# Optimization experiments

Hardware: AMD Instinct MI355X
Metric: run time of the kernel (lower is better)

The kernel has to match this reference:

```python
import jax, jax.numpy as jnp
import numpy as np

LN_EPS = 1e-9

def _layer_norm(x, g, b):
    mu = jnp.mean(x, axis=-1, keepdims=True)
    var = jnp.mean((x - mu) ** 2, axis=-1, keepdims=True)
    return (x - mu) * jax.lax.rsqrt(var + LN_EPS) * g + b

def _ffn(x, w1, b1, w2, b2, ln_g, ln_b):
    h = jax.nn.gelu(x @ w1 + b1, approximate=False)
    h = h @ w2 + b2
    return _layer_norm(h, ln_g, ln_b)

def _kernel_mean(x, y):
    d = x.shape[1]
    x2 = jnp.sum(x * x, axis=1)[:, None]
    y2 = jnp.sum(y * y, axis=1)[None, :]
    sq = x2 + y2 - 2.0 * (x @ y.T)  # [Nx, Ny]
    return jnp.mean(jnp.exp(-sq / (d * d)))

def _mmd(x, y):
    return _kernel_mean(x, x) + _kernel_mean(y, y) - 2.0 * _kernel_mean(x, y)

def setup_inputs() -> dict:
    key = jax.random.key(0)
    ks = jax.random.split(key, 8)
    B, S, D, DI, DL = 8, 512, 1024, 4096, 64
    s = lambda fan: 1.0 / np.sqrt(fan)
    return {
        "hidden": jax.random.normal(ks[0], (B, S, D), jnp.float32),
        "true_samples": jax.random.normal(ks[1], (B * S, DL), jnp.float32),
        "enc_w1": jax.random.normal(ks[2], (D, DI), jnp.float32) * s(D),
        "enc_b1": jnp.zeros((DI,), jnp.float32),
        "enc_w2": jax.random.normal(ks[3], (DI, DL), jnp.float32) * s(DI),
        "enc_b2": jnp.zeros((DL,), jnp.float32),
        "enc_ln_g": jnp.ones((DL,), jnp.float32),
        "enc_ln_b": jnp.zeros((DL,), jnp.float32),
        "dec_w1": jax.random.normal(ks[4], (DL, DI), jnp.float32) * s(DL),
        "dec_b1": jnp.zeros((DI,), jnp.float32),
        "dec_w2": jax.random.normal(ks[5], (DI, D), jnp.float32) * s(DI),
        "dec_b2": jnp.zeros((D,), jnp.float32),
        "dec_ln_g": jnp.ones((D,), jnp.float32),
        "dec_ln_b": jnp.zeros((D,), jnp.float32),
    }

def reference(hidden, true_samples, enc_w1, enc_b1, enc_w2, enc_b2, enc_ln_g, enc_ln_b,
              dec_w1, dec_b1, dec_w2, dec_b2, dec_ln_g, dec_ln_b):
    latent = _ffn(hidden, enc_w1, enc_b1, enc_w2, enc_b2, enc_ln_g, enc_ln_b)  # [B,S,DL]
    recon = _ffn(latent, dec_w1, dec_b1, dec_w2, dec_b2, dec_ln_g, dec_ln_b)   # [B,S,D]
    B, S, DL = latent.shape
    lat_flat = latent.reshape(-1, DL)  # [B*S, DL]
    reg_loss = _mmd(true_samples, lat_flat) / B * S
    return recon, latent, reg_loss
```

## Files before the change

kernel.cpp:

```cpp
#include <hip/hip_runtime.h>
#include <hip/hip_bf16.h>
#include <math.h>


typedef __attribute__((ext_vector_type(8))) short short8;
typedef __attribute__((ext_vector_type(4))) float float4a;
typedef __attribute__((ext_vector_type(4))) unsigned short us4;

__device__ inline ushort bf16r(float x) {
    union { float f; unsigned u; } c; c.f = x;
    unsigned r = (c.u + 0x7fffu + ((c.u >> 16) & 1u)) >> 16;
    return (ushort)r;
}

__device__ inline void gld_lds16(const void* g, void* l) {
    __builtin_amdgcn_global_load_lds(
        (const __attribute__((address_space(1))) void*)g,
        (__attribute__((address_space(3))) void*)l, 16, 0, 0);
}

template <int N> __device__ inline void wait_vmcnt() {
    if constexpr (N == 0) asm volatile("s_waitcnt vmcnt(0)" ::: "memory");
    else if constexpr (N == 4) asm volatile("s_waitcnt vmcnt(4)" ::: "memory");
    else if constexpr (N == 6) asm volatile("s_waitcnt vmcnt(6)" ::: "memory");
}

__device__ inline float fast_gelu(float v) {
    float v2 = v * v;
    float u = v * __builtin_fmaf(0.07135481627f, v2, 1.5957691216f);
    u = fminf(u, 30.0f);
    float e = __expf(u);
    return v * e * __builtin_amdgcn_rcpf(e + 1.0f);
}

__global__ __launch_bounds__(256) void k_pre(
        const float* __restrict__ hidden, ushort* __restrict__ A1bf,
        const float* __restrict__ tsamp, ushort* __restrict__ Tbf,
        float* __restrict__ sq_t, float* __restrict__ acc,
        const float* __restrict__ i0, ushort* __restrict__ o0,
        const float* __restrict__ i1, ushort* __restrict__ o1,
        const float* __restrict__ i2, ushort* __restrict__ o2,
        const float* __restrict__ i3, ushort* __restrict__ o3) {
    int b = blockIdx.x, tid = threadIdx.x;
    if (b == 0 && tid < 24) acc[tid] = 0.0f;
    if (b < 4096) {
        int i = b * 1024 + tid * 4;
        float4 v = *(const float4*)(hidden + i);
        us4 o = {bf16r(v.x), bf16r(v.y), bf16r(v.z), bf16r(v.w)};
        *(us4*)(A1bf + i) = o;
        return;
    }
    if (b < 4352) {
        int i = (b - 4096) * 1024 + tid * 4;
        float4 v = *(const float4*)(tsamp + i);
        us4 o = {bf16r(v.x), bf16r(v.y), bf16r(v.z), bf16r(v.w)};
        *(us4*)(Tbf + i) = o;
        float s = v.x * v.x + v.y * v.y + v.z * v.z + v.w * v.w;
#pragma unroll
        for (int off = 8; off; off >>= 1) s += __shfl_xor(s, off);
        if ((tid & 15) == 0) sq_t[i >> 6] = s;
        return;
    }
    __shared__ float t[32][33];
    const float* in; ushort* out; int R, C, lb;
    if (b < 8448)      { in = i0; out = o0; R = 1024; C = 4096; lb = b - 4352; }
    else if (b < 8704) { in = i1; out = o1; R = 4096; C = 64;   lb = b - 8448; }
    else if (b < 8960) { in = i2; out = o2; R = 64;   C = 4096; lb = b - 8704; }
    else               { in = i3; out = o3; R = 4096; C = 1024; lb = b - 8960; }
    int bx = (lb % (C / 32)) * 32;
    int by = (lb / (C / 32)) * 32;
    int tx = tid & 31, ty = tid >> 5;
#pragma unroll
    for (int i = 0; i < 32; i += 8)
        t[ty + i][tx] = in[(size_t)(by + ty + i) * C + (bx + tx)];
    __syncthreads();
#pragma unroll
    for (int i = 0; i < 32; i += 8)
        out[(size_t)(bx + ty + i) * R + (by + tx)] = bf16r(t[tx][ty + i]);
}

template <int BN, int EPI, bool SWZ>
__global__ __launch_bounds__(256) void k_gemm(
        const ushort* __restrict__ A, const ushort* __restrict__ Bt,
        const float* __restrict__ bias, void* __restrict__ Out,
        float* __restrict__ Out2, int M, int N, int K, int KC) {
    constexpr int BM = 128, BK = 64;
    constexpr int WAVES_N = BN / 64;
    constexpr int WAVES_M = 4 / WAVES_N;
    constexpr int WM = BM / WAVES_M;
    constexpr int MT = WM / 16;
    constexpr int NT = 4;
    constexpr int CA = BM / 32, CB = BN / 32;

    __shared__ ushort sA[BM * 64];
    __shared__ ushort sB[BN * 64];

    const int tid  = threadIdx.x;
    const int wave = tid >> 6, lane = tid & 63;
    const int wm = wave / WAVES_N, wn = wave % WAVES_N;
    int bx = blockIdx.x, by = blockIdx.y;
    if constexpr (SWZ) {
        int lin = blockIdx.x + gridDim.x * blockIdx.y;
        by = lin % gridDim.y;
        bx = lin / gridDim.y;
    }
    const int m0 = by * BM, n0 = bx * BN;
    const int lrow = lane & 15, lq = lane >> 4;
    const int srow8 = lane >> 3;
    const int sk8   = lane & 7;
    const int kbeg = blockIdx.z * KC;

    const ushort* pA[CA]; unsigned lA[CA];
#pragma unroll
    for (int j = 0; j < CA; ++j) {
        int c = wave * CA + j;
        int r = c * 8 + srow8;
        pA[j] = &A[(size_t)(m0 + r) * K + kbeg + ((sk8 ^ (r & 7)) * 8)];
        lA[j] = c * 512;
    }
    const ushort* pB[CB]; unsigned lB[CB];
#pragma unroll
    for (int j = 0; j < CB; ++j) {
        int c = wave * CB + j;
        int r = c * 8 + srow8;
        pB[j] = &Bt[(size_t)(n0 + r) * K + kbeg + ((sk8 ^ (r & 7)) * 8)];
        lB[j] = c * 512;
    }
    unsigned aoff[2][MT], boff[2][NT];
#pragma unroll
    for (int h = 0; h < 2; ++h) {
#pragma unroll
        for (int mt = 0; mt < MT; ++mt) {
            int r = wm * WM + mt * 16 + lrow;
            aoff[h][mt] = r * 64 + (((h * 4 + lq) ^ (r & 7)) * 8);
        }
#pragma unroll
        for (int nt = 0; nt < NT; ++nt) {
            int r = wn * 64 + nt * 16 + lrow;
            boff[h][nt] = r * 64 + (((h * 4 + lq) ^ (r & 7)) * 8);
        }
    }

    float4a acc[MT][NT];
#pragma unroll
    for (int mt = 0; mt < MT; ++mt)
#pragma unroll
        for (int nt = 0; nt < NT; ++nt)
            acc[mt][nt] = (float4a){0.f, 0.f, 0.f, 0.f};

    for (int k0 = 0; k0 < KC; k0 += BK) {
#pragma unroll
        for (int j = 0; j < CA; ++j) {
            gld_lds16(pA[j], &sA[lA[j]]);
            pA[j] += BK;
        }
#pragma unroll
        for (int j = 0; j < CB; ++j) {
            gld_lds16(pB[j], &sB[lB[j]]);
            pB[j] += BK;
        }
        __syncthreads();
#pragma unroll
        for (int h = 0; h < 2; ++h) {
            short8 af[MT], bfr[NT];
#pragma unroll
            for (int mt = 0; mt < MT; ++mt)
                af[mt] = *(short8*)(&sA[aoff[h][mt]]);
#pragma unroll
            for (int nt = 0; nt < NT; ++nt)
                bfr[nt] = *(short8*)(&sB[boff[h][nt]]);
#pragma unroll
            for (int mt = 0; mt < MT; ++mt)
#pragma unroll
                for (int nt = 0; nt < NT; ++nt)
                    acc[mt][nt] = __builtin_amdgcn_mfma_f32_16x16x32_bf16(
                        af[mt], bfr[nt], acc[mt][nt], 0, 0, 0);
        }
        __syncthreads();
    }

    float* dstp = nullptr;
    if constexpr (EPI == 2) {
        if (Out2 && blockIdx.z) dstp = Out2;
        else dstp = (float*)Out + (size_t)blockIdx.z * M * N;
    }
#pragma unroll
    for (int mt = 0; mt < MT; ++mt)
#pragma unroll
        for (int nt = 0; nt < NT; ++nt) {
            int col = n0 + wn * 64 + nt * 16 + lrow;
            float bv = 0.f;
            if constexpr (EPI != 2) bv = bias[col];
#pragma unroll
            for (int r = 0; r < 4; ++r) {
                int row = m0 + wm * WM + mt * 16 + lq * 4 + r;
                float v = acc[mt][nt][r] + bv;
                if constexpr (EPI == 0) {
                    ((ushort*)Out)[(size_t)row * N + col] = bf16r(fast_gelu(v));
                } else if constexpr (EPI == 1) {
                    ((float*)Out)[(size_t)row * N + col] = v;
                } else {
                    dstp[(size_t)row * N + col] = v;
                }
            }
        }
}

template <int BN, int EPI, int CX, int CY>
__global__ __launch_bounds__(512, 2) void k_gemm256(
        const ushort* __restrict__ A, const ushort* __restrict__ Bt,
        const float* __restrict__ bias, void* __restrict__ Out,
        float* __restrict__ Out2, int M, int N, int K, int KC) {
    constexpr int BM = 256, BK = 64;
    constexpr int AI = 4;
    constexpr int BI = BN / 64;
    constexpr int BLO = (BN == 256) ? 2 : 0;
    constexpr int WAVES_N = BN / 64;
    constexpr int WAVES_M = 8 / WAVES_N;
    constexpr int WM = BM / WAVES_M;
    constexpr int MT = WM / 16;
    constexpr int NT = 4;
    constexpr int PH = MT / 2;
    constexpr int INF = AI + BLO;

    __shared__ ushort sA[2][BM * 64];
    __shared__ ushort sB[2][BN * 64];

    const int tid = threadIdx.x;
    const int wave = tid >> 6, lane = tid & 63;
    const int wm = wave / WAVES_N, wn = wave % WAVES_N;

    const int gx = gridDim.x, gy = gridDim.y;
    const int lin = blockIdx.x + gx * (blockIdx.y + gy * blockIdx.z);
    const int nwg = gx * gy * gridDim.z;
    const int cpx = nwg >> 3;
    const int swz = (lin & 7) * cpx + (lin >> 3);
    const int nz  = gx * gy;
    const int zz  = swz / nz;
    const int rr  = swz % nz;
    const int chunk = rr / (CX * CY);
    const int lcl   = rr % (CX * CY);
    const int ncx   = gx / CX;
    const int bx = (chunk % ncx) * CX + (lcl % CX);
    const int by = (chunk / ncx) * CY + (lcl / CX);

    const int m0 = by * BM, n0 = bx * BN;
    const int lrow = lane & 15, lq = lane >> 4;
    const int kbeg = zz * KC;
    const int nT = KC / BK;

    const int crow = tid >> 3;
    const int ck8  = (tid & 7) ^ (crow & 7);
    const ushort* pAbase = A  + (size_t)(m0 + crow) * K + kbeg + ck8 * 8;
    const ushort* pBbase = Bt + (size_t)(n0 + crow) * K + kbeg + ck8 * 8;

    const int a0  = (wm * WM + lrow) * 64;
    const int b0  = (wn * 64 + lrow) * 64;
    const int sw0 = ((lq) ^ (lrow & 7)) * 8;
    const int sw1 = ((4 + lq) ^ (lrow & 7)) * 8;

    float4a acc[MT][NT];
#pragma unroll
    for (int mt = 0; mt < MT; ++mt)
#pragma unroll
        for (int nt = 0; nt < NT; ++nt)
            acc[mt][nt] = (float4a){0.f, 0.f, 0.f, 0.f};

#pragma unroll
    for (int j = 0; j < AI; ++j)
        gld_lds16(pAbase + (size_t)j * 64 * K, &sA[0][j * 4096 + wave * 512]);
#pragma unroll
    for (int j = 0; j < BI; ++j)
        gld_lds16(pBbase + (size_t)j * 64 * K, &sB[0][j * 4096 + wave * 512]);
    if (nT > 1) {
#pragma unroll
        for (int j = 0; j < AI; ++j)
            gld_lds16(pAbase + (size_t)j * 64 * K + BK,
                      &sA[1][j * 4096 + wave * 512]);
#pragma unroll
        for (int j = 0; j < BLO; ++j)
            gld_lds16(pBbase + (size_t)j * 64 * K + BK,
                      &sB[1][j * 4096 + wave * 512]);
        wait_vmcnt<INF>();
    } else {
        wait_vmcnt<0>();
    }
    __builtin_amdgcn_s_barrier();
    __builtin_amdgcn_sched_barrier(0);

    short8 bfr[2][NT];

    for (int t = 0; t < nT; ++t) {
        const int d = t & 1;
        const bool pf1 = (t + 1 < nT), pf2 = (t + 2 < nT);
        const size_t koff1 = (size_t)(t + 1) * BK;
        const size_t koff2 = (size_t)(t + 2) * BK;

#pragma unroll
        for (int q = 0; q < PH; ++q) {
            short8 af[2][2];
#pragma unroll
            for (int i = 0; i < 2; ++i) {
                af[0][i] = *(const short8*)(&sA[d][a0 + (q * 2 + i) * 1024 + sw0]);
                af[1][i] = *(const short8*)(&sA[d][a0 + (q * 2 + i) * 1024 + sw1]);
            }
            if (q == 0) {
#pragma unroll
                for (int nt = 0; nt < NT; ++nt) {
                    bfr[0][nt] = *(const short8*)(&sB[d][b0 + nt * 1024 + sw0]);
                    bfr[1][nt] = *(const short8*)(&sB[d][b0 + nt * 1024 + sw1]);
                }
                if (pf1) {
#pragma unroll
                    for (int j = BLO; j < BLO + 2; ++j)
                        gld_lds16(pBbase + (size_t)j * 64 * K + koff1,
                                  &sB[d ^ 1][j * 4096 + wave * 512]);
                }
            }
            __builtin_amdgcn_s_barrier();
            asm volatile("s_waitcnt lgkmcnt(0)" ::: "memory");
            __builtin_amdgcn_sched_barrier(0);
            __builtin_amdgcn_s_setprio(1);
#pragma unroll
            for (int h = 0; h < 2; ++h)
#pragma unroll
                for (int i = 0; i < 2; ++i)
#pragma unroll
                    for (int nt = 0; nt < NT; ++nt)
                        acc[q * 2 + i][nt] =
                            __builtin_amdgcn_mfma_f32_16x16x32_bf16(
                                af[h][i], bfr[h][nt], acc[q * 2 + i][nt],
                                0, 0, 0);
            __builtin_amdgcn_s_setprio(0);
            __builtin_amdgcn_sched_barrier(0);
            __builtin_amdgcn_s_barrier();
            __builtin_amdgcn_sched_barrier(0);
        }
        if (pf2) {
#pragma unroll
            for (int j = 0; j < AI; ++j)
                gld_lds16(pAbase + (size_t)j * 64 * K + koff2,
                          &sA[d][j * 4096 + wave * 512]);
#pragma unroll
            for (int j = 0; j < BLO; ++j)
                gld_lds16(pBbase + (size_t)j * 64 * K + koff2,
                          &sB[d][j * 4096 + wave * 512]);
        }
        if (pf1) {
            if (pf2) wait_vmcnt<INF>();
            else     wait_vmcnt<0>();
            __builtin_amdgcn_s_barrier();
            __builtin_amdgcn_sched_barrier(0);
        }
    }

    float* dstp = nullptr;
    if constexpr (EPI == 2) {
        if (Out2 && zz) dstp = Out2;
        else dstp = (float*)Out + (size_t)zz * M * N;
    }
#pragma unroll
    for (int mt = 0; mt < MT; ++mt)
#pragma unroll
        for (int nt = 0; nt < NT; ++nt) {
            const int col = n0 + wn * 64 + nt * 16 + lrow;
            float bv = 0.f;
            if constexpr (EPI == 0) bv = bias[col];
#pragma unroll
            for (int r = 0; r < 4; ++r) {
                const int row = m0 + wm * WM + mt * 16 + lq * 4 + r;
                float v = acc[mt][nt][r] + bv;
                if constexpr (EPI == 0)
                    ((ushort*)Out)[(size_t)row * N + col] = bf16r(fast_gelu(v));
                else
                    dstp[(size_t)row * N + col] = v;
            }
        }
}

__global__ __launch_bounds__(256) void k_gram_all(
        const ushort* __restrict__ Tbf, const ushort* __restrict__ Lbf,
        const float* __restrict__ sq_t, const float* __restrict__ sq_l,
        float* __restrict__ accum) {
    __shared__ ushort sX[128 * 64];
    __shared__ ushort sY[128 * 64];
    __shared__ float red[4];

    int id = blockIdx.x;
    int pair, tbx, tby; float w;
    if (id < 1056) {
        pair = (id < 528) ? 0 : 1;
        int t = (pair == 0) ? id : id - 528;
        int r = (int)((sqrtf(8.0f * t + 1.0f) - 1.0f) * 0.5f);
        while ((r + 1) * (r + 2) / 2 <= t) ++r;
        while (r * (r + 1) / 2 > t) --r;
        tby = r; tbx = t - r * (r + 1) / 2;
        w = (tbx == tby) ? 1.0f : 2.0f;
    } else {
        pair = 2; int t = id - 1056;
        tbx = t & 31; tby = t >> 5; w = 1.0f;
    }
    const ushort* Xb = (pair == 1) ? Lbf : Tbf;
    const ushort* Yb = (pair == 0) ? Tbf : Lbf;
    const float* sqX = (pair == 1) ? sq_l : sq_t;
    const float* sqY = (pair == 0) ? sq_t : sq_l;

    const int tid  = threadIdx.x;
    const int wave = tid >> 6, lane = tid & 63;
    const int wm = wave >> 1, wn = wave & 1;
    const int bx = tbx * 128, by = tby * 128;
    const int lrow = lane & 15, lq = lane >> 4;
    const int srow8 = lane >> 3, sk8 = lane & 7;

#pragma unroll
    for (int j = 0; j < 4; ++j) {
        int c = wave * 4 + j;
        int r = c * 8 + srow8;
        int kc = (sk8 ^ (r & 7)) * 8;
        gld_lds16(&Xb[(size_t)(bx + r) * 64 + kc], &sX[c * 512]);
        gld_lds16(&Yb[(size_t)(by + r) * 64 + kc], &sY[c * 512]);
    }

    unsigned xoff[2][4], yoff[2][4];
#pragma unroll
    for (int h = 0; h < 2; ++h)
#pragma unroll
        for (int i = 0; i < 4; ++i) {
            int rx = wm * 64 + i * 16 + lrow;
            int ry = wn * 64 + i * 16 + lrow;
            xoff[h][i] = rx * 64 + (((h * 4 + lq) ^ (rx & 7)) * 8);
            yoff[h][i] = ry * 64 + (((h * 4 + lq) ^ (ry & 7)) * 8);
        }
    __syncthreads();

    float4a acc[4][4];
#pragma unroll
    for (int mt = 0; mt < 4; ++mt)
#pragma unroll
        for (int nt = 0; nt < 4; ++nt)
            acc[mt][nt] = (float4a){0.f, 0.f, 0.f, 0.f};

#pragma unroll
    for (int h = 0; h < 2; ++h) {
        short8 xf[4], yf[4];
#pragma unroll
        for (int mt = 0; mt < 4; ++mt)
            xf[mt] = *(short8*)(&sX[xoff[h][mt]]);
#pragma unroll
        for (int nt = 0; nt < 4; ++nt)
            yf[nt] = *(short8*)(&sY[yoff[h][nt]]);
#pragma unroll
        for (int mt = 0; mt < 4; ++mt)
#pragma unroll
            for (int nt = 0; nt < 4; ++nt)
                acc[mt][nt] = __builtin_amdgcn_mfma_f32_16x16x32_bf16(
                    xf[mt], yf[nt], acc[mt][nt], 0, 0, 0);
    }

    float sy[4];
#pragma unroll
    for (int nt = 0; nt < 4; ++nt)
        sy[nt] = sqY[by + wn * 64 + nt * 16 + lrow];
    float s = 0.f;
#pragma unroll
    for (int mt = 0; mt < 4; ++mt)
#pragma unroll
        for (int r = 0; r < 4; ++r) {
            float sx = sqX[bx + wm * 64 + mt * 16 + lq * 4 + r];
#pragma unroll
            for (int nt = 0; nt < 4; ++nt)
                s += __expf((2.0f * acc[mt][nt][r] - sx - sy[nt]) * (1.0f / 4096.0f));
        }
    s *= w;
#pragma unroll
    for (int off = 32; off; off >>= 1) s += __shfl_xor(s, off);
    if ((tid & 63) == 0) red[tid >> 6] = s;
    __syncthreads();
    if (tid == 0) atomicAdd(accum + pair * 8, red[0] + red[1] + red[2] + red[3]);
}

__global__ __launch_bounds__(256) void k_ln64_red(
        const float* __restrict__ part, int npart,
        const float* __restrict__ bias, const float* __restrict__ g,
        const float* __restrict__ b, float* __restrict__ outf,
        ushort* __restrict__ outb, float* __restrict__ sq_l) {
    int wave = threadIdx.x >> 6, lane = threadIdx.x & 63;
    int row = blockIdx.x * 4 + wave;
    float x = bias[lane];
    for (int s = 0; s < npart; ++s)
        x += part[(size_t)s * 4096 * 64 + row * 64 + lane];
    float s = x;
#pragma unroll
    for (int off = 32; off; off >>= 1) s += __shfl_xor(s, off);
    float mu = s * (1.0f / 64.0f);
    float d = x - mu;
    float v = d * d;
#pragma unroll
    for (int off = 32; off; off >>= 1) v += __shfl_xor(v, off);
    float rs = rsqrtf(v * (1.0f / 64.0f) + 1e-9f);
    float y = d * rs * g[lane] + b[lane];
    outf[row * 64 + lane] = y;
    outb[row * 64 + lane] = bf16r(y);
    float q = y * y;
#pragma unroll
    for (int off = 32; off; off >>= 1) q += __shfl_xor(q, off);
    if (lane == 0) sq_l[row] = q;
}

__global__ __launch_bounds__(256) void k_ln1024_red(
        const float* __restrict__ p0, const float* __restrict__ p1,
        const float* __restrict__ bias, const float* __restrict__ g,
        const float* __restrict__ b, float* __restrict__ out) {
    __shared__ float red[4];
    int row = blockIdx.x, tid = threadIdx.x;
    const float4 v0 = *(const float4*)(p0 + (size_t)row * 1024 + tid * 4);
    const float4 v1 = *(const float4*)(p1 + (size_t)row * 1024 + tid * 4);
    const float4 bb = *(const float4*)(bias + tid * 4);
    float4 v;
    v.x = v0.x + v1.x + bb.x;
    v.y = v0.y + v1.y + bb.y;
    v.z = v0.z + v1.z + bb.z;
    v.w = v0.w + v1.w + bb.w;
    float s = v.x + v.y + v.z + v.w;
#pragma unroll
    for (int off = 32; off; off >>= 1) s += __shfl_xor(s, off);
    if ((tid & 63) == 0) red[tid >> 6] = s;
    __syncthreads();
    float mu = (red[0] + red[1] + red[2] + red[3]) * (1.0f / 1024.0f);
    float dx = v.x - mu, dy = v.y - mu, dz = v.z - mu, dw = v.w - mu;
    float q = dx * dx + dy * dy + dz * dz + dw * dw;
#pragma unroll
    for (int off = 32; off; off >>= 1) q += __shfl_xor(q, off);
    __syncthreads();
    if ((tid & 63) == 0) red[tid >> 6] = q;
    __syncthreads();
    float rs = rsqrtf((red[0] + red[1] + red[2] + red[3]) * (1.0f / 1024.0f) + 1e-9f);
    const float4 gv = *(const float4*)(g + tid * 4);
    const float4 bv = *(const float4*)(b + tid * 4);
    float4 o;
    o.x = dx * rs * gv.x + bv.x;
    o.y = dy * rs * gv.y + bv.y;
    o.z = dz * rs * gv.z + bv.z;
    o.w = dw * rs * gv.w + bv.w;
    *(float4*)(out + (size_t)row * 1024 + tid * 4) = o;
}

__global__ void k_finalize(const float* __restrict__ accum, float* __restrict__ out) {
    out[0] = (accum[0] + accum[8] - 2.0f * accum[16]) * (64.0f / (4096.0f * 4096.0f));
}

extern "C" void kernel_launch(void* const* d_in, const int* in_sizes, int n_in,
                              void* d_out, int out_size, void* d_ws, size_t ws_size,
                              hipStream_t stream) {
    const float* hidden   = (const float*)d_in[0];
    const float* tsamp    = (const float*)d_in[1];
    const float* enc_w1   = (const float*)d_in[2];
    const float* enc_b1   = (const float*)d_in[3];
    const float* enc_w2   = (const float*)d_in[4];
    const float* enc_b2   = (const float*)d_in[5];
    const float* enc_ln_g = (const float*)d_in[6];
    const float* enc_ln_b = (const float*)d_in[7];
    const float* dec_w1   = (const float*)d_in[8];
    const float* dec_b1   = (const float*)d_in[9];
    const float* dec_w2   = (const float*)d_in[10];
    const float* dec_b2   = (const float*)d_in[11];
    const float* dec_ln_g = (const float*)d_in[12];
    const float* dec_ln_b = (const float*)d_in[13];

    float* out      = (float*)d_out;
    float* recon    = out;
    float* latent_f = out + 4194304;
    float* reg      = out + 4456448;

    char* ws = (char*)d_ws;
    const size_t MB = 1024 * 1024;
    ushort* A1bf = (ushort*)(ws + 0);
    ushort* W1t  = (ushort*)(ws + 8 * MB);
    float*  part = (float*)(ws + 0);
    float*  h4p0 = (float*)(ws + 0);
    ushort* H1bf = (ushort*)(ws + 16 * MB);
    ushort* W4t  = (ushort*)(ws + 48 * MB);
    ushort* W2t  = (ushort*)(ws + 56 * MB);
    ushort* W3t  = (ushort*)(ws + 56 * MB + 512 * 1024);
    ushort* Lbf  = (ushort*)(ws + 57 * MB);
    float*  sq_t = (float*)(ws + 59 * MB);
    float*  sq_l = (float*)(ws + 59 * MB + 16384);
    float*  acc3 = (float*)(ws + 59 * MB + 32768);
    ushort* Tbf  = (ushort*)(ws + 59 * MB + 65536);

    k_pre<<<13056, 256, 0, stream>>>(hidden, A1bf, tsamp, Tbf, sq_t, acc3,
                                     enc_w1, W1t, enc_w2, W2t,
                                     dec_w1, W3t, dec_w2, W4t);

    k_gemm256<256, 0, 4, 8><<<dim3(16, 16, 1), 512, 0, stream>>>(
        A1bf, W1t, enc_b1, H1bf, nullptr, 4096, 4096, 1024, 1024);
    k_gemm<64, 2, false><<<dim3(1, 32, 16), 256, 0, stream>>>(
        H1bf, W2t, nullptr, part, nullptr, 4096, 64, 4096, 256);
    k_ln64_red<<<1024, 256, 0, stream>>>(part, 16, enc_b2, enc_ln_g, enc_ln_b,
                                         latent_f, Lbf, sq_l);

    k_gemm<64, 0, false><<<dim3(64, 32, 1), 256, 0, stream>>>(
        Lbf, W3t, dec_b1, H1bf, nullptr, 4096, 4096, 64, 64);
    k_gemm256<128, 2, 8, 4><<<dim3(8, 16, 2), 512, 0, stream>>>(
        H1bf, W4t, nullptr, h4p0, recon, 4096, 1024, 4096, 2048);
    k_ln1024_red<<<4096, 256, 0, stream>>>(h4p0, recon, dec_b2, dec_ln_g,
                                           dec_ln_b, recon);

    k_gram_all<<<2080, 256, 0, stream>>>(Tbf, Lbf, sq_t, sq_l, acc3);
    k_finalize<<<1, 1, 0, stream>>>(acc3, reg);
}
```

Before: 275.1 us.

## Restructure GEMM main loop to single-stage prefetch with split LDS waits

Replaces the two-tile-ahead prefetch with per-phase barriers by a simpler loop. Each iteration reads all A/B fragments for both K halves from LDS, issues the next tile's global-to-LDS loads into the other buffer, waits on lgkmcnt for the first half, runs its MFMAs, then waits for the rest and runs the second half. This drops the per-phase barriers and overlaps LDS reads with MFMA work. In exchange, global prefetch now runs only one tile ahead with a full vmcnt(0) wait every iteration, which may expose more memory latency. It also holds more fragment registers live.

```diff
diff --git a/kernel.cpp b/kernel.cpp
--- a/kernel.cpp
+++ b/kernel.cpp
@@ -23,6 +23,12 @@
     if constexpr (N == 0) asm volatile("s_waitcnt vmcnt(0)" ::: "memory");
     else if constexpr (N == 4) asm volatile("s_waitcnt vmcnt(4)" ::: "memory");
     else if constexpr (N == 6) asm volatile("s_waitcnt vmcnt(6)" ::: "memory");
+}
+
+template <int N> __device__ inline void wait_lgkmcnt() {
+    if constexpr (N == 0) asm volatile("s_waitcnt lgkmcnt(0)" ::: "memory");
+    else if constexpr (N == 8) asm volatile("s_waitcnt lgkmcnt(8)" ::: "memory");
+    else if constexpr (N == 12) asm volatile("s_waitcnt lgkmcnt(12)" ::: "memory");
 }
 
 __device__ inline float fast_gelu(float v) {
@@ -214,14 +220,11 @@
     constexpr int BM = 256, BK = 64;
     constexpr int AI = 4;
     constexpr int BI = BN / 64;
-    constexpr int BLO = (BN == 256) ? 2 : 0;
     constexpr int WAVES_N = BN / 64;
     constexpr int WAVES_M = 8 / WAVES_N;
     constexpr int WM = BM / WAVES_M;
     constexpr int MT = WM / 16;
     constexpr int NT = 4;
-    constexpr int PH = MT / 2;
-    constexpr int INF = AI + BLO;
 
     __shared__ ushort sA[2][BM * 64];
     __shared__ ushort sB[2][BN * 64];
@@ -272,83 +275,61 @@
 #pragma unroll
     for (int j = 0; j < BI; ++j)
         gld_lds16(pBbase + (size_t)j * 64 * K, &sB[0][j * 4096 + wave * 512]);
-    if (nT > 1) {
-#pragma unroll
-        for (int j = 0; j < AI; ++j)
-            gld_lds16(pAbase + (size_t)j * 64 * K + BK,
-                      &sA[1][j * 4096 + wave * 512]);
-#pragma unroll
-        for (int j = 0; j < BLO; ++j)
-            gld_lds16(pBbase + (size_t)j * 64 * K + BK,
-                      &sB[1][j * 4096 + wave * 512]);
-        wait_vmcnt<INF>();
-    } else {
-        wait_vmcnt<0>();
-    }
+    wait_vmcnt<0>();
     __builtin_amdgcn_s_barrier();
     __builtin_amdgcn_sched_barrier(0);
 
-    short8 bfr[2][NT];
-
     for (int t = 0; t < nT; ++t) {
         const int d = t & 1;
-        const bool pf1 = (t + 1 < nT), pf2 = (t + 2 < nT);
+        const bool pf1 = (t + 1 < nT);
         const size_t koff1 = (size_t)(t + 1) * BK;
-        const size_t koff2 = (size_t)(t + 2) * BK;
-
-#pragma unroll
-        for (int q = 0; q < PH; ++q) {
-            short8 af[2][2];
-#pragma unroll
-            for (int i = 0; i < 2; ++i) {
-                af[0][i] = *(const short8*)(&sA[d][a0 + (q * 2 + i) * 1024 + sw0]);
-                af[1][i] = *(const short8*)(&sA[d][a0 + (q * 2 + i) * 1024 + sw1]);
-            }
-            if (q == 0) {
-#pragma unroll
-                for (int nt = 0; nt < NT; ++nt) {
-                    bfr[0][nt] = *(const short8*)(&sB[d][b0 + nt * 1024 + sw0]);
-                    bfr[1][nt] = *(const short8*)(&sB[d][b0 + nt * 1024 + sw1]);
-                }
-                if (pf1) {
-#pragma unroll
-                    for (int j = BLO; j < BLO + 2; ++j)
-                        gld_lds16(pBbase + (size_t)j * 64 * K + koff1,
-                                  &sB[d ^ 1][j * 4096 + wave * 512]);
-                }
-            }
-            __builtin_amdgcn_s_barrier();
-            asm volatile("s_waitcnt lgkmcnt(0)" ::: "memory");
-            __builtin_amdgcn_sched_barrier(0);
-            __builtin_amdgcn_s_setprio(1);
-#pragma unroll
-            for (int h = 0; h < 2; ++h)
-#pragma unroll
-                for (int i = 0; i < 2; ++i)
-#pragma unroll
-                    for (int nt = 0; nt < NT; ++nt)
-                        acc[q * 2 + i][nt] =
-                            __builtin_amdgcn_mfma_f32_16x16x32_bf16(
-                                af[h][i], bfr[h][nt], acc[q * 2 + i][nt],
-                                0, 0, 0);
-            __builtin_amdgcn_s_setprio(0);
-            __builtin_amdgcn_sched_barrier(0);
-            __builtin_amdgcn_s_barrier();
-            __builtin_amdgcn_sched_barrier(0);
-        }
-        if (pf2) {
+
+        short8 af0[MT], bfr0[NT], af1[MT], bfr1[NT];
+#pragma unroll
+        for (int mt = 0; mt < MT; ++mt)
+            af0[mt] = *(const short8*)(&sA[d][a0 + mt * 1024 + sw0]);
+#pragma unroll
+        for (int nt = 0; nt < NT; ++nt)
+            bfr0[nt] = *(const short8*)(&sB[d][b0 + nt * 1024 + sw0]);
+        __builtin_amdgcn_sched_barrier(0);
+#pragma unroll
+        for (int mt = 0; mt < MT; ++mt)
+            af1[mt] = *(const short8*)(&sA[d][a0 + mt * 1024 + sw1]);
+#pragma unroll
+        for (int nt = 0; nt < NT; ++nt)
+            bfr1[nt] = *(const short8*)(&sB[d][b0 + nt * 1024 + sw1]);
+        if (pf1) {
 #pragma unroll
             for (int j = 0; j < AI; ++j)
-                gld_lds16(pAbase + (size_t)j * 64 * K + koff2,
-                          &sA[d][j * 4096 + wave * 512]);
-#pragma unroll
-            for (int j = 0; j < BLO; ++j)
-                gld_lds16(pBbase + (size_t)j * 64 * K + koff2,
-                          &sB[d][j * 4096 + wave * 512]);
-        }
+                gld_lds16(pAbase + (size_t)j * 64 * K + koff1,
+                          &sA[d ^ 1][j * 4096 + wave * 512]);
+#pragma unroll
+            for (int j = 0; j < BI; ++j)
+                gld_lds16(pBbase + (size_t)j * 64 * K + koff1,
+                          &sB[d ^ 1][j * 4096 + wave * 512]);
+        }
+        wait_lgkmcnt<MT + 4>();
+        __builtin_amdgcn_sched_barrier(0);
+        __builtin_amdgcn_s_setprio(1);
+#pragma unroll
+        for (int mt = 0; mt < MT; ++mt)
+#pragma unroll
+            for (int nt = 0; nt < NT; ++nt)
+                acc[mt][nt] = __builtin_amdgcn_mfma_f32_16x16x32_bf16(
+                    af0[mt], bfr0[nt], acc[mt][nt], 0, 0, 0);
+        __builtin_amdgcn_s_setprio(0);
+        wait_lgkmcnt<0>();
+        __builtin_amdgcn_sched_barrier(0);
+        __builtin_amdgcn_s_setprio(1);
+#pragma unroll
+        for (int mt = 0; mt < MT; ++mt)
+#pragma unroll
+            for (int nt = 0; nt < NT; ++nt)
+                acc[mt][nt] = __builtin_amdgcn_mfma_f32_16x16x32_bf16(
+                    af1[mt], bfr1[nt], acc[mt][nt], 0, 0, 0);
+        __builtin_amdgcn_s_setprio(0);
         if (pf1) {
-            if (pf2) wait_vmcnt<INF>();
-            else     wait_vmcnt<0>();
+            wait_vmcnt<0>();
             __builtin_amdgcn_s_barrier();
             __builtin_amdgcn_sched_barrier(0);
         }
```

Result: faster. 263.7 us (-4.1%).
